# Kernel tuning notes

Measured on AMD Instinct MI355X. Metric: run time of the kernel, lower is better.

## Reference

```python
import jax, jax.numpy as jnp
import numpy as np

N_HEADS = 8  # must match init_kwargs n_heads


def _shift(x, dy, dx):
    """out[..., y, x] = x[..., y+dy, x+dx], zero-padded outside. Replaces im2col gather / col2im scatter."""
    H, W = x.shape[-2], x.shape[-1]
    py0, py1 = max(dy, 0), max(-dy, 0)
    px0, px1 = max(dx, 0), max(-dx, 0)
    xp = jnp.pad(x, [(0, 0)] * (x.ndim - 2) + [(py1, py0), (px1, px0)])
    return xp[..., py1 + dy:py1 + dy + H, px1 + dx:px1 + dx + W]


def setup_inputs() -> dict:
    key = jax.random.key(0)
    k1, k2, k3 = jax.random.split(key, 3)
    N, D, H, W = 8, 256, 128, 128
    V = jax.random.normal(k1, (N, D, H, W), dtype=jnp.float32)
    K = jax.random.normal(k2, (N, D, H, W), dtype=jnp.float32)
    Q = jax.random.normal(k3, (N, D, H, W), dtype=jnp.float32)
    mask = jnp.ones((N, 1, H, W), dtype=jnp.float32)
    return {"V": V, "K": K, "Q": Q, "ksize": 5, "dilation": 1, "mask": mask}


def reference(V, K, Q, ksize, dilation, mask):
    N, D, H, W = Q.shape
    Dv = V.shape[1]
    nh = N_HEADS
    h_dim = D // nh
    dv_h = Dv // nh
    pad = (ksize // 2) * dilation
    offsets = [(i * dilation - pad, j * dilation - pad)
               for i in range(ksize) for j in range(ksize)]  # P = ksize**2 window positions

    # per-head QK scores for each window offset: score_p = sum_c K[y+dy, x+dx] * Q[y, x]
    Qh = Q.reshape(N, nh, h_dim, H, W)
    scores = []
    for (dy, dx) in offsets:
        Ks = _shift(K, dy, dx).reshape(N, nh, h_dim, H, W)
        scores.append(jnp.sum(Ks * Qh, axis=2))  # (N, nh, H, W)
    scores = jnp.stack(scores, axis=0)  # (P, N, nh, H, W)

    # softmax over window positions (dim 2 in the torch code), then mask
    att = jax.nn.softmax(scores, axis=0)
    m = mask.reshape(N, 1, H, W)[:, 0]  # (N, H, W)
    att = att * m[None, :, None, :, :]

    # diffuse V: value at (y, x) weighted by att[p] scatters to (y+dy, x+dx) (col2im add)
    Vh = V.reshape(N, nh, dv_h, H, W)
    out = jnp.zeros((N, nh, dv_h, H, W), dtype=V.dtype)
    for p, (dy, dx) in enumerate(offsets):
        contrib = Vh * att[p][:, :, None]  # (N, nh, dv_h, H, W)
        out = out + _shift(contrib, -dy, -dx)
    return out.reshape(N, Dv, H, W)
```

## Files before the change

kernel.cpp:

```cpp
#include <hip/hip_runtime.h>
#include <hip/hip_bf16.h>

typedef __hip_bfloat16 bf16;
typedef __attribute__((ext_vector_type(2))) __fp16    fp16x2;
typedef __attribute__((ext_vector_type(2))) _Float16  half2t;

#define N_     8
#define NH     8
#define HD     32
#define HW     (128 * 128)
#define H_     128
#define W_     128
#define P_     25
#define NPLANE (N_ * NH * HW)

#define ATY    4
#define ARG    8
#define APITCH 136
#define CH     4
#define NCH    (HD / CH)

#define TY     8
#define RG     12
#define PITCH  136

static __device__ __forceinline__ unsigned short f2bf(float f) {
  bf16 b = __float2bfloat16(f);
  return *(unsigned short*)&b;
}
union h2u { unsigned u; fp16x2 f; half2t h; };
static __device__ __forceinline__ unsigned pk2u(float a, float b) {
  h2u x; x.f = __builtin_amdgcn_cvt_pkrtz(a, b); return x.u;
}
static __device__ __forceinline__ half2t u2h(unsigned v) {
  h2u x; x.u = v; return x.h;
}

__global__ __launch_bounds__(256) void attn_kernel(
    const float* __restrict__ Kp, const float* __restrict__ Qp,
    const float* __restrict__ maskp, bf16* __restrict__ att) {
  __shared__ unsigned Lh[2][ARG][APITCH];

  const int tid = threadIdx.x;
  const int y0 = blockIdx.x * ATY, nh = blockIdx.y;
  const int ty = tid >> 6, g = tid & 63;
  const int gy = y0 + ty, gx0 = 2 * g;
  const float* KU = Kp + (size_t)nh * (HD * HW);
  const float* QU = Qp + (size_t)nh * (HD * HW);
  const int qidx = gy * W_ + gx0;

  const int scol = tid & 127;
  const int sr0  = tid >> 7;
  int gofs[4]; bool okr[4];
#pragma unroll
  for (int j = 0; j < 4; ++j) {
    const int ky = y0 - 2 + sr0 + 2 * j;
    okr[j] = (unsigned)ky < H_;
    gofs[j] = okr[j] ? ky * W_ + scol : 0;
  }

  if (tid < 64) {
    const int m = tid >> 5, rem = tid & 31, r = rem >> 2, c = rem & 3;
    Lh[m][r][c < 2 ? c : c + 128] = 0u;
  }

  float s[P_][2];
#pragma unroll
  for (int p = 0; p < P_; ++p) { s[p][0] = 0.f; s[p][1] = 0.f; }

  const float2 mv = *(const float2*)(maskp + (size_t)(nh >> 3) * HW + qidx);

#pragma unroll 1
  for (int kc = 0; kc < NCH; ++kc) {
    const int cb = kc * CH;
    if (kc) __syncthreads();

    float t[4][CH];
#pragma unroll
    for (int j = 0; j < 4; ++j)
#pragma unroll
      for (int c = 0; c < CH; ++c)
        t[j][c] = okr[j] ? KU[gofs[j] + (cb + c) * HW] : 0.f;
#pragma unroll
    for (int j = 0; j < 4; ++j)
#pragma unroll
      for (int m = 0; m < 2; ++m)
        Lh[m][sr0 + 2 * j][scol + 2] = pk2u(t[j][2 * m], t[j][2 * m + 1]);
    __syncthreads();

    float2 qv[CH];
#pragma unroll
    for (int c = 0; c < CH; ++c)
      qv[c] = *(const float2*)(QU + (cb + c) * HW + qidx);
    unsigned qp[2][2];
#pragma unroll
    for (int m = 0; m < 2; ++m) {
      qp[m][0] = pk2u(qv[2 * m].x, qv[2 * m + 1].x);
      qp[m][1] = pk2u(qv[2 * m].y, qv[2 * m + 1].y);
    }

#pragma unroll
    for (int m = 0; m < 2; ++m)
#pragma unroll
      for (int dyi = 0; dyi < 5; ++dyi) {
        const unsigned* rp = &Lh[m][ty + dyi][2 * g];
        uint2 a = *(const uint2*)rp;
        uint2 b = *(const uint2*)(rp + 2);
        uint2 c = *(const uint2*)(rp + 4);
        unsigned r[6] = {a.x, a.y, b.x, b.y, c.x, c.y};
#pragma unroll
        for (int dxi = 0; dxi < 5; ++dxi) {
          s[dyi * 5 + dxi][0] = __builtin_amdgcn_fdot2(
              u2h(r[dxi]),     u2h(qp[m][0]), s[dyi * 5 + dxi][0], false);
          s[dyi * 5 + dxi][1] = __builtin_amdgcn_fdot2(
              u2h(r[dxi + 1]), u2h(qp[m][1]), s[dyi * 5 + dxi][1], false);
        }
      }
  }

  float inv[2];
#pragma unroll
  for (int px = 0; px < 2; ++px) {
    float m = s[0][px];
#pragma unroll
    for (int p = 1; p < P_; ++p) m = fmaxf(m, s[p][px]);
    float sum = 0.f;
#pragma unroll
    for (int p = 0; p < P_; ++p) { float e = __expf(s[p][px] - m); s[p][px] = e; sum += e; }
    inv[px] = (px ? mv.y : mv.x) / sum;
  }
  unsigned short* A = (unsigned short*)att;
  const size_t pixbase = (size_t)nh * HW + qidx;
#pragma unroll
  for (int p = 0; p < P_; ++p) {
    unsigned o = (unsigned)f2bf(s[p][0] * inv[0]) |
                 ((unsigned)f2bf(s[p][1] * inv[1]) << 16);
    *(unsigned*)(A + (size_t)p * NPLANE + pixbase) = o;
  }
}

#define DCH 4
#define DNCH (HD / DCH)
__global__ __launch_bounds__(256) void diffuse_kernel(
    const float* __restrict__ Vp, const bf16* __restrict__ att,
    float* __restrict__ out) {
  __shared__ float L[DCH][RG][PITCH];

  const int tid = threadIdx.x;
  const int y0 = blockIdx.x * TY, nh = blockIdx.y;
  const int ty = tid >> 5, g = tid & 31;
  const int gy = y0 + ty, gx0 = 4 * g;
  const float* VU = Vp + (size_t)nh * (HD * HW);
  float* OU = out + (size_t)nh * (HD * HW);

  const int scol = tid & 127;
  const int sr0  = tid >> 7;
  int gofs[6]; bool okr[6];
#pragma unroll
  for (int j = 0; j < 6; ++j) {
    const int ky = y0 - 2 + sr0 + 2 * j;
    okr[j] = (unsigned)ky < H_;
    gofs[j] = okr[j] ? ky * W_ + scol : 0;
  }

  float t[6][DCH];
#pragma unroll
  for (int j = 0; j < 6; ++j)
#pragma unroll
    for (int ch = 0; ch < DCH; ++ch)
      t[j][ch] = okr[j] ? VU[gofs[j] + ch * HW] : 0.f;

  const unsigned short* A = (const unsigned short*)att;
  unsigned mxl[5], mxh[5];
#pragma unroll
  for (int exi = 0; exi < 5; ++exi) {
    bool o0 = (unsigned)(gx0 + 0 + exi - 2) < W_;
    bool o1 = (unsigned)(gx0 + 1 + exi - 2) < W_;
    bool o2 = (unsigned)(gx0 + 2 + exi - 2) < W_;
    bool o3 = (unsigned)(gx0 + 3 + exi - 2) < W_;
    mxl[exi] = (o0 ? 0xFFFFu : 0u) | (o1 ? 0xFFFF0000u : 0u);
    mxh[exi] = (o2 ? 0xFFFFu : 0u) | (o3 ? 0xFFFF0000u : 0u);
  }
  uint2 wp[P_];
#pragma unroll
  for (int j = 0; j < P_; ++j) {
    const int eyi = j / 5, exi = j % 5;
    const int ys = gy + eyi - 2;
    uint2 v; v.x = 0u; v.y = 0u;
    if ((unsigned)ys < H_) {
      const size_t base = (size_t)(24 - j) * NPLANE + (size_t)nh * HW +
                          (size_t)(ys * W_) + (gx0 + exi - 2);
      if (exi == 2) {
        v = *(const uint2*)(A + base);
      } else if ((exi & 1) == 0) {
        v.x = *(const unsigned*)(A + base);
        v.y = *(const unsigned*)(A + base + 2);
      } else {
        unsigned u0 = *(const unsigned*)(A + base - 1);
        unsigned u1 = *(const unsigned*)(A + base + 1);
        unsigned u2 = *(const unsigned*)(A + base + 3);
        v.x = (u0 >> 16) | (u1 << 16);
        v.y = (u1 >> 16) | (u2 << 16);
      }
    }
    v.x &= mxl[exi]; v.y &= mxh[exi];
    wp[j] = v;
  }

  if (tid < 192) {
    const int ch = tid / 48, rem = tid % 48, r = rem >> 2, c = rem & 3;
    L[ch][r][c < 2 ? c : c + 128] = 0.f;
  }

#pragma unroll 1
  for (int kc = 0; kc < DNCH; ++kc) {
    if (kc) __syncthreads();
#pragma unroll
    for (int j = 0; j < 6; ++j)
#pragma unroll
      for (int ch = 0; ch < DCH; ++ch)
        L[ch][sr0 + 2 * j][scol + 2] = t[j][ch];
    __syncthreads();

    if (kc < DNCH - 1) {
      const int cn = (kc + 1) * DCH;
#pragma unroll
      for (int j = 0; j < 6; ++j)
#pragma unroll
        for (int ch = 0; ch < DCH; ++ch)
          t[j][ch] = okr[j] ? VU[gofs[j] + (cn + ch) * HW] : 0.f;
    }

    float acc[DCH][4];
#pragma unroll
    for (int ch = 0; ch < DCH; ++ch)
#pragma unroll
      for (int px = 0; px < 4; ++px) acc[ch][px] = 0.f;

#pragma unroll
    for (int eyi = 0; eyi < 5; ++eyi) {
      float vr[DCH][8];
#pragma unroll
      for (int ch = 0; ch < DCH; ++ch) {
        const float* rp = &L[ch][ty + eyi][4 * g];
        float4 ra = *(const float4*)rp;
        float4 rb = *(const float4*)(rp + 4);
        vr[ch][0] = ra.x; vr[ch][1] = ra.y; vr[ch][2] = ra.z; vr[ch][3] = ra.w;
        vr[ch][4] = rb.x; vr[ch][5] = rb.y; vr[ch][6] = rb.z; vr[ch][7] = rb.w;
      }
#pragma unroll
      for (int exi = 0; exi < 5; ++exi) {
        const uint2 w2 = wp[eyi * 5 + exi];
        float wf[4];
        wf[0] = __uint_as_float(w2.x << 16);
        wf[1] = __uint_as_float(w2.x & 0xFFFF0000u);
        wf[2] = __uint_as_float(w2.y << 16);
        wf[3] = __uint_as_float(w2.y & 0xFFFF0000u);
#pragma unroll
        for (int ch = 0; ch < DCH; ++ch)
#pragma unroll
          for (int px = 0; px < 4; ++px)
            acc[ch][px] += wf[px] * vr[ch][px + exi];
      }
    }

    const int c0 = kc * DCH;
#pragma unroll
    for (int ch = 0; ch < DCH; ++ch) {
      float4 o = make_float4(acc[ch][0], acc[ch][1], acc[ch][2], acc[ch][3]);
      *(float4*)(OU + (c0 + ch) * HW + gy * W_ + gx0) = o;
    }
  }
}

extern "C" void kernel_launch(void* const* d_in, const int* in_sizes, int n_in,
                              void* d_out, int out_size, void* d_ws, size_t ws_size,
                              hipStream_t stream) {
  const float* V    = (const float*)d_in[0];
  const float* K    = (const float*)d_in[1];
  const float* Q    = (const float*)d_in[2];
  const float* mask = (const float*)d_in[5];

  bf16* att = (bf16*)d_ws;

  dim3 gridA(H_ / ATY, N_ * NH);
  attn_kernel<<<gridA, 256, 0, stream>>>(K, Q, mask, att);
  dim3 gridB(H_ / TY, N_ * NH);
  diffuse_kernel<<<gridB, 256, 0, stream>>>(V, att, (float*)d_out);
}
```

Measured before the change: 166.6 us.

## Split attention into score and softmax kernels, staging all K channels in LDS

The fused attention kernel is split into a score kernel and a separate softmax kernel. The score kernel loads all 32 K channels into shared memory once and holds all Q pairs in registers. It then computes scores one window row at a time, so it keeps only 10 accumulators instead of 50, and writes raw fp16 scores to the workspace. A separate elementwise softmax kernel reads those scores back, applies softmax and the mask, and rewrites bf16 weights in place. This removes the per-chunk barriers and lowers register pressure, but adds an extra launch and a full read and write of the score buffer. Scores are also now rounded to fp16 before the softmax.

```diff
diff --git a/kernel.cpp b/kernel.cpp
--- a/kernel.cpp
+++ b/kernel.cpp
@@ -13,16 +13,17 @@
 #define W_     128
 #define P_     25
 #define NPLANE (N_ * NH * HW)
-
-#define ATY    4
-#define ARG    8
-#define APITCH 136
-#define CH     4
-#define NCH    (HD / CH)
+#define NPD    (NPLANE / 2)
+
+#define SY     4
+#define SRG    8
+#define SPITCH 136
 
 #define TY     8
 #define RG     12
 #define PITCH  136
+#define DCH    4
+#define DNCH   (HD / DCH)
 
 static __device__ __forceinline__ unsigned short f2bf(float f) {
   bf16 b = __float2bfloat16(f);
@@ -36,13 +37,13 @@
   h2u x; x.u = v; return x.h;
 }
 
-__global__ __launch_bounds__(256) void attn_kernel(
+__global__ __launch_bounds__(256) void score_kernel(
     const float* __restrict__ Kp, const float* __restrict__ Qp,
-    const float* __restrict__ maskp, bf16* __restrict__ att) {
-  __shared__ unsigned Lh[2][ARG][APITCH];
+    unsigned* __restrict__ araw) {
+  __shared__ unsigned Lh[16][SRG][SPITCH];
 
   const int tid = threadIdx.x;
-  const int y0 = blockIdx.x * ATY, nh = blockIdx.y;
+  const int y0 = blockIdx.x * SY, nh = blockIdx.y;
   const int ty = tid >> 6, g = tid & 63;
   const int gy = y0 + ty, gx0 = 2 * g;
   const float* KU = Kp + (size_t)nh * (HD * HW);
@@ -59,88 +60,98 @@
     gofs[j] = okr[j] ? ky * W_ + scol : 0;
   }
 
-  if (tid < 64) {
-    const int m = tid >> 5, rem = tid & 31, r = rem >> 2, c = rem & 3;
-    Lh[m][r][c < 2 ? c : c + 128] = 0u;
-  }
-
-  float s[P_][2];
-#pragma unroll
-  for (int p = 0; p < P_; ++p) { s[p][0] = 0.f; s[p][1] = 0.f; }
-
-  const float2 mv = *(const float2*)(maskp + (size_t)(nh >> 3) * HW + qidx);
+#pragma unroll
+  for (int i = 0; i < 2; ++i) {
+    const int id = tid + 256 * i;
+    const int cp = id >> 5, rem = id & 31, r = rem >> 2, c = rem & 3;
+    Lh[cp][r][c < 2 ? c : c + 128] = 0u;
+  }
+
+  unsigned qp[16][2];
+#pragma unroll
+  for (int cp = 0; cp < 16; ++cp) {
+    float2 a = *(const float2*)(QU + (2 * cp) * HW + qidx);
+    float2 b = *(const float2*)(QU + (2 * cp + 1) * HW + qidx);
+    qp[cp][0] = pk2u(a.x, b.x);
+    qp[cp][1] = pk2u(a.y, b.y);
+  }
 
 #pragma unroll 1
-  for (int kc = 0; kc < NCH; ++kc) {
-    const int cb = kc * CH;
-    if (kc) __syncthreads();
-
-    float t[4][CH];
+  for (int grp = 0; grp < 8; ++grp) {
+    const int cb = 4 * grp;
+    float t[4][4];
 #pragma unroll
     for (int j = 0; j < 4; ++j)
 #pragma unroll
-      for (int c = 0; c < CH; ++c)
+      for (int c = 0; c < 4; ++c)
         t[j][c] = okr[j] ? KU[gofs[j] + (cb + c) * HW] : 0.f;
 #pragma unroll
     for (int j = 0; j < 4; ++j)
 #pragma unroll
       for (int m = 0; m < 2; ++m)
-        Lh[m][sr0 + 2 * j][scol + 2] = pk2u(t[j][2 * m], t[j][2 * m + 1]);
-    __syncthreads();
-
-    float2 qv[CH];
-#pragma unroll
-    for (int c = 0; c < CH; ++c)
-      qv[c] = *(const float2*)(QU + (cb + c) * HW + qidx);
-    unsigned qp[2][2];
-#pragma unroll
-    for (int m = 0; m < 2; ++m) {
-      qp[m][0] = pk2u(qv[2 * m].x, qv[2 * m + 1].x);
-      qp[m][1] = pk2u(qv[2 * m].y, qv[2 * m + 1].y);
-    }
-
-#pragma unroll
-    for (int m = 0; m < 2; ++m)
-#pragma unroll
-      for (int dyi = 0; dyi < 5; ++dyi) {
-        const unsigned* rp = &Lh[m][ty + dyi][2 * g];
-        uint2 a = *(const uint2*)rp;
-        uint2 b = *(const uint2*)(rp + 2);
-        uint2 c = *(const uint2*)(rp + 4);
-        unsigned r[6] = {a.x, a.y, b.x, b.y, c.x, c.y};
-#pragma unroll
-        for (int dxi = 0; dxi < 5; ++dxi) {
-          s[dyi * 5 + dxi][0] = __builtin_amdgcn_fdot2(
-              u2h(r[dxi]),     u2h(qp[m][0]), s[dyi * 5 + dxi][0], false);
-          s[dyi * 5 + dxi][1] = __builtin_amdgcn_fdot2(
-              u2h(r[dxi + 1]), u2h(qp[m][1]), s[dyi * 5 + dxi][1], false);
-        }
+        Lh[2 * grp + m][sr0 + 2 * j][scol + 2] = pk2u(t[j][2 * m], t[j][2 * m + 1]);
+  }
+  __syncthreads();
+
+  unsigned* ap = araw + (((size_t)nh * HW + qidx) >> 1);
+
+#pragma unroll
+  for (int dy = 0; dy < 5; ++dy) {
+    float s0[5], s1[5];
+#pragma unroll
+    for (int dx = 0; dx < 5; ++dx) { s0[dx] = 0.f; s1[dx] = 0.f; }
+#pragma unroll
+    for (int cp = 0; cp < 16; ++cp) {
+      const unsigned* rp = &Lh[cp][ty + dy][2 * g];
+      uint2 a = *(const uint2*)rp;
+      uint2 b = *(const uint2*)(rp + 2);
+      uint2 c = *(const uint2*)(rp + 4);
+      unsigned r[6] = {a.x, a.y, b.x, b.y, c.x, c.y};
+#pragma unroll
+      for (int dx = 0; dx < 5; ++dx) {
+        s0[dx] = __builtin_amdgcn_fdot2(u2h(r[dx]),     u2h(qp[cp][0]), s0[dx], false);
+        s1[dx] = __builtin_amdgcn_fdot2(u2h(r[dx + 1]), u2h(qp[cp][1]), s1[dx], false);
       }
-  }
-
-  float inv[2];
-#pragma unroll
-  for (int px = 0; px < 2; ++px) {
-    float m = s[0][px];
-#pragma unroll
-    for (int p = 1; p < P_; ++p) m = fmaxf(m, s[p][px]);
-    float sum = 0.f;
-#pragma unroll
-    for (int p = 0; p < P_; ++p) { float e = __expf(s[p][px] - m); s[p][px] = e; sum += e; }
-    inv[px] = (px ? mv.y : mv.x) / sum;
-  }
-  unsigned short* A = (unsigned short*)att;
-  const size_t pixbase = (size_t)nh * HW + qidx;
+    }
+#pragma unroll
+    for (int dx = 0; dx < 5; ++dx)
+      ap[(size_t)(dy * 5 + dx) * NPD] = pk2u(s0[dx], s1[dx]);
+  }
+}
+
+__global__ __launch_bounds__(256) void softmax_kernel(
+    unsigned* __restrict__ att, const float* __restrict__ maskp) {
+  const int idx = blockIdx.x * 256 + threadIdx.x;
+
+  unsigned v[P_];
+#pragma unroll
+  for (int p = 0; p < P_; ++p) v[p] = att[(size_t)p * NPD + idx];
+
+  float e0[P_], e1[P_];
+  float m0 = -1e30f, m1 = -1e30f;
 #pragma unroll
   for (int p = 0; p < P_; ++p) {
-    unsigned o = (unsigned)f2bf(s[p][0] * inv[0]) |
-                 ((unsigned)f2bf(s[p][1] * inv[1]) << 16);
-    *(unsigned*)(A + (size_t)p * NPLANE + pixbase) = o;
-  }
-}
-
-#define DCH 4
-#define DNCH (HD / DCH)
+    half2t h = u2h(v[p]);
+    e0[p] = (float)h[0]; e1[p] = (float)h[1];
+    m0 = fmaxf(m0, e0[p]); m1 = fmaxf(m1, e1[p]);
+  }
+  float sum0 = 0.f, sum1 = 0.f;
+#pragma unroll
+  for (int p = 0; p < P_; ++p) {
+    e0[p] = __expf(e0[p] - m0); sum0 += e0[p];
+    e1[p] = __expf(e1[p] - m1); sum1 += e1[p];
+  }
+  const int pix2 = idx * 2;
+  const int nh = pix2 / HW;
+  const int pix = pix2 & (HW - 1);
+  const float2 mv = *(const float2*)(maskp + (size_t)(nh >> 3) * HW + pix);
+  const float i0 = mv.x / sum0, i1 = mv.y / sum1;
+#pragma unroll
+  for (int p = 0; p < P_; ++p)
+    att[(size_t)p * NPD + idx] =
+        (unsigned)f2bf(e0[p] * i0) | ((unsigned)f2bf(e1[p] * i1) << 16);
+}
+
 __global__ __launch_bounds__(256) void diffuse_kernel(
     const float* __restrict__ Vp, const bf16* __restrict__ att,
     float* __restrict__ out) {
@@ -281,10 +292,11 @@
   const float* Q    = (const float*)d_in[2];
   const float* mask = (const float*)d_in[5];
 
-  bf16* att = (bf16*)d_ws;
-
-  dim3 gridA(H_ / ATY, N_ * NH);
-  attn_kernel<<<gridA, 256, 0, stream>>>(K, Q, mask, att);
+  unsigned* att = (unsigned*)d_ws;
+
+  dim3 gridS(H_ / SY, N_ * NH);
+  score_kernel<<<gridS, 256, 0, stream>>>(K, Q, att);
+  softmax_kernel<<<NPD / 256, 256, 0, stream>>>(att, mask);
   dim3 gridB(H_ / TY, N_ * NH);
-  diffuse_kernel<<<gridB, 256, 0, stream>>>(V, att, (float*)d_out);
-}
+  diffuse_kernel<<<gridB, 256, 0, stream>>>(V, (const bf16*)att, (float*)d_out);
+}
```

Result: slower. 190.9 us (+14.5%).

## Compute attention scores with bf16 MFMA over a staged K window

Applied to the files above, without the earlier changes.

Rewrites the score kernel to stage all 32 head channels of K for an 8-row halo into LDS as packed bf16. Scores are then computed with 16x16x32 bf16 MFMA instructions instead of per-pixel fp16 dot2 loops. Blocks grow to 512 threads and the softmax drops max-subtraction, masking out invalid window positions in the MFMA tile. This trades wasted MFMA lanes, narrower bf16 precision, scattered 2-byte attention stores and a larger LDS footprint for far fewer ALU instructions. Skipping the max risks overflow for large scores.

```diff
diff --git a/kernel.cpp b/kernel.cpp
--- a/kernel.cpp
+++ b/kernel.cpp
@@ -2,8 +2,8 @@
 #include <hip/hip_bf16.h>
 
 typedef __hip_bfloat16 bf16;
-typedef __attribute__((ext_vector_type(2))) __fp16    fp16x2;
-typedef __attribute__((ext_vector_type(2))) _Float16  half2t;
+typedef __attribute__((ext_vector_type(8))) short bf16x8;
+typedef __attribute__((ext_vector_type(4))) float f32x4;
 
 #define N_     8
 #define NH     8
@@ -14,133 +14,151 @@
 #define P_     25
 #define NPLANE (N_ * NH * HW)
 
-#define ATY    4
-#define ARG    8
-#define APITCH 136
-#define CH     4
-#define NCH    (HD / CH)
+#define AROWS  4
+#define KROWS  8
+#define KCOLS  132
+#define KPITCH 18
 
 #define TY     8
 #define RG     12
 #define PITCH  136
+#define DCH    4
+#define DNCH   (HD / DCH)
 
 static __device__ __forceinline__ unsigned short f2bf(float f) {
   bf16 b = __float2bfloat16(f);
   return *(unsigned short*)&b;
 }
-union h2u { unsigned u; fp16x2 f; half2t h; };
-static __device__ __forceinline__ unsigned pk2u(float a, float b) {
-  h2u x; x.f = __builtin_amdgcn_cvt_pkrtz(a, b); return x.u;
-}
-static __device__ __forceinline__ half2t u2h(unsigned v) {
-  h2u x; x.u = v; return x.h;
-}
-
-__global__ __launch_bounds__(256) void attn_kernel(
+static __device__ __forceinline__ unsigned pkbf(float a, float b) {
+  return (unsigned)f2bf(a) | ((unsigned)f2bf(b) << 16);
+}
+union abf { unsigned u[4]; bf16x8 v; };
+
+__global__ __launch_bounds__(512) void attn_kernel(
     const float* __restrict__ Kp, const float* __restrict__ Qp,
-    const float* __restrict__ maskp, bf16* __restrict__ att) {
-  __shared__ unsigned Lh[2][ARG][APITCH];
+    const float* __restrict__ maskp, unsigned short* __restrict__ att) {
+  __shared__ unsigned KlF[KROWS * KCOLS * KPITCH];
 
   const int tid = threadIdx.x;
-  const int y0 = blockIdx.x * ATY, nh = blockIdx.y;
-  const int ty = tid >> 6, g = tid & 63;
-  const int gy = y0 + ty, gx0 = 2 * g;
+  const int y0 = blockIdx.x * AROWS, nh = blockIdx.y;
   const float* KU = Kp + (size_t)nh * (HD * HW);
   const float* QU = Qp + (size_t)nh * (HD * HW);
-  const int qidx = gy * W_ + gx0;
-
-  const int scol = tid & 127;
-  const int sr0  = tid >> 7;
-  int gofs[4]; bool okr[4];
-#pragma unroll
-  for (int j = 0; j < 4; ++j) {
-    const int ky = y0 - 2 + sr0 + 2 * j;
-    okr[j] = (unsigned)ky < H_;
-    gofs[j] = okr[j] ? ky * W_ + scol : 0;
-  }
-
-  if (tid < 64) {
-    const int m = tid >> 5, rem = tid & 31, r = rem >> 2, c = rem & 3;
-    Lh[m][r][c < 2 ? c : c + 128] = 0u;
-  }
-
-  float s[P_][2];
-#pragma unroll
-  for (int p = 0; p < P_; ++p) { s[p][0] = 0.f; s[p][1] = 0.f; }
-
-  const float2 mv = *(const float2*)(maskp + (size_t)(nh >> 3) * HW + qidx);
-
-#pragma unroll 1
-  for (int kc = 0; kc < NCH; ++kc) {
-    const int cb = kc * CH;
-    if (kc) __syncthreads();
-
-    float t[4][CH];
-#pragma unroll
-    for (int j = 0; j < 4; ++j)
-#pragma unroll
-      for (int c = 0; c < CH; ++c)
-        t[j][c] = okr[j] ? KU[gofs[j] + (cb + c) * HW] : 0.f;
-#pragma unroll
-    for (int j = 0; j < 4; ++j)
-#pragma unroll
-      for (int m = 0; m < 2; ++m)
-        Lh[m][sr0 + 2 * j][scol + 2] = pk2u(t[j][2 * m], t[j][2 * m + 1]);
-    __syncthreads();
-
-    float2 qv[CH];
-#pragma unroll
-    for (int c = 0; c < CH; ++c)
-      qv[c] = *(const float2*)(QU + (cb + c) * HW + qidx);
-    unsigned qp[2][2];
-#pragma unroll
-    for (int m = 0; m < 2; ++m) {
-      qp[m][0] = pk2u(qv[2 * m].x, qv[2 * m + 1].x);
-      qp[m][1] = pk2u(qv[2 * m].y, qv[2 * m + 1].y);
-    }
-
-#pragma unroll
-    for (int m = 0; m < 2; ++m)
-#pragma unroll
-      for (int dyi = 0; dyi < 5; ++dyi) {
-        const unsigned* rp = &Lh[m][ty + dyi][2 * g];
-        uint2 a = *(const uint2*)rp;
-        uint2 b = *(const uint2*)(rp + 2);
-        uint2 c = *(const uint2*)(rp + 4);
-        unsigned r[6] = {a.x, a.y, b.x, b.y, c.x, c.y};
-#pragma unroll
-        for (int dxi = 0; dxi < 5; ++dxi) {
-          s[dyi * 5 + dxi][0] = __builtin_amdgcn_fdot2(
-              u2h(r[dxi]),     u2h(qp[m][0]), s[dyi * 5 + dxi][0], false);
-          s[dyi * 5 + dxi][1] = __builtin_amdgcn_fdot2(
-              u2h(r[dxi + 1]), u2h(qp[m][1]), s[dyi * 5 + dxi][1], false);
+
+  const int w = tid >> 6, l = tid & 63;
+  const int ry = w >> 1;
+  const int gyq = y0 + ry;
+  const int q = l & 15, grp = l >> 4, g4 = 4 * grp;
+  const int qxbase = (w & 1) * 64;
+
+  {
+    const int pc = tid & 3, rem = tid >> 2;
+    const int zr = rem >> 4, zd = rem & 15;
+    const int zc = pc < 2 ? pc : pc + 128;
+    KlF[(zr * KCOLS + zc) * KPITCH + zd] = 0u;
+  }
+
+#pragma unroll
+  for (int i = 0; i < 2; ++i) {
+    const int pid = tid + 512 * i;
+    const int row = pid >> 7, col = pid & 127;
+    const int gyk = y0 - 2 + row;
+    const bool ok = (unsigned)gyk < H_;
+    const float* src = KU + (ok ? gyk * W_ + col : 0);
+    unsigned kp[16];
+#pragma unroll
+    for (int m = 0; m < 16; ++m) {
+      float a = ok ? src[(2 * m) * HW] : 0.f;
+      float b = ok ? src[(2 * m + 1) * HW] : 0.f;
+      kp[m] = pkbf(a, b);
+    }
+    unsigned* dst = &KlF[(row * KCOLS + col + 2) * KPITCH];
+#pragma unroll
+    for (int e = 0; e < 8; ++e)
+      *(uint2*)(dst + 2 * e) = make_uint2(kp[2 * e], kp[2 * e + 1]);
+  }
+
+  bf16x8 bfr[4];
+  float maskv[4];
+#pragma unroll
+  for (int s = 0; s < 4; ++s) {
+    const int qc = qxbase + 16 * s + q;
+    const float* qsrc = QU + (8 * grp) * HW + gyq * W_ + qc;
+    abf u;
+#pragma unroll
+    for (int e = 0; e < 4; ++e)
+      u.u[e] = pkbf(qsrc[(2 * e) * HW], qsrc[(2 * e + 1) * HW]);
+    bfr[s] = u.v;
+    maskv[s] = maskp[(size_t)(nh >> 3) * HW + gyq * W_ + qc];
+  }
+
+  int abase[7];
+#pragma unroll
+  for (int t = 0; t < 7; ++t) {
+    int f = 16 * t + q;
+    int dyr = f / 20;
+    int kc = f - 20 * dyr;
+    int rowK = ry + dyr; if (rowK > 7) rowK = 7;
+    abase[t] = (rowK * KCOLS + kc) * KPITCH + g4;
+  }
+
+  __syncthreads();
+
+  unsigned short* A16 = att + (size_t)nh * HW + gyq * W_;
+
+#pragma unroll
+  for (int s = 0; s < 4; ++s) {
+    const int qx0 = qxbase + 16 * s;
+    const int qc = qx0 + q;
+
+    f32x4 acc[7];
+#pragma unroll
+    for (int t = 0; t < 7; ++t) {
+      const unsigned* ap = &KlF[abase[t] + qx0 * KPITCH];
+      uint2 lo = *(const uint2*)ap;
+      uint2 hi = *(const uint2*)(ap + 2);
+      abf ua; ua.u[0] = lo.x; ua.u[1] = lo.y; ua.u[2] = hi.x; ua.u[3] = hi.y;
+      acc[t] = __builtin_amdgcn_mfma_f32_16x16x32_bf16(
+          ua.v, bfr[s], (f32x4){0.f, 0.f, 0.f, 0.f}, 0, 0, 0);
+    }
+
+    float spart = 0.f;
+#pragma unroll
+    for (int t = 0; t < 7; ++t)
+#pragma unroll
+      for (int j = 0; j < 4; ++j) {
+        const int TJ = 16 * t + j;
+        int f = TJ + g4;
+        int dyr = f / 20;
+        int d = f - 20 * dyr - q;
+        bool v = (unsigned)d < 5u;
+        if (TJ >= 88) v = v && (f < 100);
+        float e = v ? __expf(acc[t][j]) : 0.f;
+        acc[t][j] = e;
+        spart += e;
+      }
+    float ssum = spart;
+    ssum += __shfl_xor(ssum, 16);
+    ssum += __shfl_xor(ssum, 32);
+    const float inv = maskv[s] / ssum;
+
+#pragma unroll
+    for (int t = 0; t < 7; ++t)
+#pragma unroll
+      for (int j = 0; j < 4; ++j) {
+        const int TJ = 16 * t + j;
+        int f = TJ + g4;
+        int dyr = f / 20;
+        int d = f - 20 * dyr - q;
+        bool v = (unsigned)d < 5u;
+        if (TJ >= 88) v = v && (f < 100);
+        if (v) {
+          int p = dyr * 5 + d;
+          A16[(size_t)p * NPLANE + qc] = f2bf(acc[t][j] * inv);
         }
       }
   }
-
-  float inv[2];
-#pragma unroll
-  for (int px = 0; px < 2; ++px) {
-    float m = s[0][px];
-#pragma unroll
-    for (int p = 1; p < P_; ++p) m = fmaxf(m, s[p][px]);
-    float sum = 0.f;
-#pragma unroll
-    for (int p = 0; p < P_; ++p) { float e = __expf(s[p][px] - m); s[p][px] = e; sum += e; }
-    inv[px] = (px ? mv.y : mv.x) / sum;
-  }
-  unsigned short* A = (unsigned short*)att;
-  const size_t pixbase = (size_t)nh * HW + qidx;
-#pragma unroll
-  for (int p = 0; p < P_; ++p) {
-    unsigned o = (unsigned)f2bf(s[p][0] * inv[0]) |
-                 ((unsigned)f2bf(s[p][1] * inv[1]) << 16);
-    *(unsigned*)(A + (size_t)p * NPLANE + pixbase) = o;
-  }
-}
-
-#define DCH 4
-#define DNCH (HD / DCH)
+}
+
 __global__ __launch_bounds__(256) void diffuse_kernel(
     const float* __restrict__ Vp, const bf16* __restrict__ att,
     float* __restrict__ out) {
@@ -281,10 +299,10 @@
   const float* Q    = (const float*)d_in[2];
   const float* mask = (const float*)d_in[5];
 
-  bf16* att = (bf16*)d_ws;
-
-  dim3 gridA(H_ / ATY, N_ * NH);
-  attn_kernel<<<gridA, 256, 0, stream>>>(K, Q, mask, att);
+  unsigned short* att = (unsigned short*)d_ws;
+
+  dim3 gridA(H_ / AROWS, N_ * NH);
+  attn_kernel<<<gridA, 512, 0, stream>>>(K, Q, mask, att);
   dim3 gridB(H_ / TY, N_ * NH);
-  diffuse_kernel<<<gridB, 256, 0, stream>>>(V, att, (float*)d_out);
-}
+  diffuse_kernel<<<gridB, 256, 0, stream>>>(V, (const bf16*)att, (float*)d_out);
+}
```

Result: slower. 372.0 us (+123.2%).
